# Performance work log

Measured on AMD Instinct MI355X. Metric: run time of the kernel, lower is better.

The kernel has to match this reference:

```python
import jax, jax.numpy as jnp
import numpy as np

PH, PW = 7, 7          # output_size
GRID = 2               # sampling_ratio
SCALES = (0.25, 0.125, 0.0625, 0.03125)  # 2^round(log2(feat/img)) per level
LVL_MIN, LVL_MAX = 2, 5                  # -log2(scales[0]), -log2(scales[-1])
CANON_SCALE, CANON_LVL = 224.0, 4.0
EPS = 1e-6


def setup_inputs() -> dict:
    key = jax.random.key(0)
    ks = jax.random.split(key, 6)
    B, C = 2, 256
    sizes = [(200, 200), (100, 100), (50, 50), (25, 25)]
    inp = {f"feat{i}": jax.random.normal(ks[i], (B, C, h, w), jnp.float32)
           for i, (h, w) in enumerate(sizes)}
    Nb = 256
    # boxes in 800x800 image coords, x1y1 + positive wh so 0<=x1<x2, 0<=y1<y2
    xy = jax.random.uniform(ks[4], (B, Nb, 2), jnp.float32, 0.0, 700.0)
    wh = jax.random.uniform(ks[5], (B, Nb, 2), jnp.float32, 32.0, 512.0)
    inp["boxes"] = jnp.concatenate([xy, xy + wh], axis=-1)
    return inp


def _roi_align_level(feat, b_idx, rois, scale):
    """torchvision roi_align, aligned=False. feat [B,C,H,W], rois [R,4] -> [R,C,PH,PW]."""
    H, W = feat.shape[2], feat.shape[3]
    x1 = rois[:, 0] * scale
    y1 = rois[:, 1] * scale
    x2 = rois[:, 2] * scale
    y2 = rois[:, 3] * scale
    roi_w = jnp.maximum(x2 - x1, 1.0)
    roi_h = jnp.maximum(y2 - y1, 1.0)
    bin_w = roi_w / PW
    bin_h = roi_h / PH
    # sub-bin sampling offsets: (bin + (i+0.5)/grid) for each bin, flattened [PH*GRID]
    gy = (jnp.arange(PH, dtype=jnp.float32)[:, None]
          + (jnp.arange(GRID, dtype=jnp.float32)[None, :] + 0.5) / GRID).reshape(-1)
    gx = (jnp.arange(PW, dtype=jnp.float32)[:, None]
          + (jnp.arange(GRID, dtype=jnp.float32)[None, :] + 0.5) / GRID).reshape(-1)
    ys = y1[:, None] + gy[None, :] * bin_h[:, None]   # [R, PH*G]
    xs = x1[:, None] + gx[None, :] * bin_w[:, None]   # [R, PW*G]
    y = ys[:, :, None]                                 # [R, PH*G, 1]
    x = xs[:, None, :]                                 # [R, 1, PW*G]
    valid = (y >= -1.0) & (y <= H) & (x >= -1.0) & (x <= W)
    yc = jnp.clip(y, 0.0, H - 1)
    xc = jnp.clip(x, 0.0, W - 1)
    yl = jnp.floor(yc).astype(jnp.int32)
    xl = jnp.floor(xc).astype(jnp.int32)
    yh = jnp.minimum(yl + 1, H - 1)
    xh = jnp.minimum(xl + 1, W - 1)
    ly = yc - yl.astype(yc.dtype)
    lx = xc - xl.astype(xc.dtype)
    hy = 1.0 - ly
    hx = 1.0 - lx
    b = b_idx[:, None, None]

    def gather(yi, xi):
        # advanced indexing with slice in channel dim -> [R, PH*G, PW*G, C]
        return feat[b, :, yi, xi]

    val = ((hy * hx)[..., None] * gather(yl, xl)
           + (hy * lx)[..., None] * gather(yl, xh)
           + (ly * hx)[..., None] * gather(yh, xl)
           + (ly * lx)[..., None] * gather(yh, xh))
    val = jnp.where(valid[..., None], val, 0.0)
    R, C = rois.shape[0], feat.shape[1]
    # average over the GRIDxGRID sampling points of each bin
    val = val.reshape(R, PH, GRID, PW, GRID, C).mean(axis=(2, 4))  # [R,PH,PW,C]
    return jnp.transpose(val, (0, 3, 1, 2))                        # [R,C,PH,PW]


def reference(feat0, feat1, feat2, feat3, boxes):
    feats = [feat0, feat1, feat2, feat3]
    B, Nb = boxes.shape[0], boxes.shape[1]
    rois = boxes.reshape(-1, 4)                               # convert_to_roi_format
    b_idx = jnp.repeat(jnp.arange(B), Nb)
    # LevelMapper (FPN eq. 1)
    s = jnp.sqrt(jnp.maximum((rois[:, 2] - rois[:, 0]) * (rois[:, 3] - rois[:, 1]), 0.0))
    lvl = jnp.floor(CANON_LVL + jnp.log2(s / CANON_SCALE + EPS))
    lvl = jnp.clip(lvl, LVL_MIN, LVL_MAX).astype(jnp.int32) - LVL_MIN  # [R] in [0,3]
    out = jnp.zeros((rois.shape[0], feats[0].shape[1], PH, PW), feats[0].dtype)
    for l, (f, sc) in enumerate(zip(feats, SCALES)):
        pooled = _roi_align_level(f, b_idx, rois, sc)
        out = jnp.where((lvl == l)[:, None, None, None], pooled, out)
    return out
```

## Files before the change

### kernel.cpp

```cpp
#include <hip/hip_runtime.h>


#define PHW 49
#define NCHUNK 8
#define CH 32
#define NC 4
#define PSIZE 1024

__global__ __launch_bounds__(256) void msroi_kernel(
    const float* __restrict__ f0, const float* __restrict__ f1,
    const float* __restrict__ f2, const float* __restrict__ f3,
    const float* __restrict__ boxes, float* __restrict__ out)
{
    const int C = 256, Nb = 256;
    const int r = blockIdx.x;
    const int chunk = blockIdx.y;
    const int tid = threadIdx.x;
    const int b = r / Nb;

    const float x1b = boxes[r * 4 + 0];
    const float y1b = boxes[r * 4 + 1];
    const float x2b = boxes[r * 4 + 2];
    const float y2b = boxes[r * 4 + 3];
    const float area = fmaxf((x2b - x1b) * (y2b - y1b), 0.0f);
    const float s = sqrtf(area);
    float lv = floorf(4.0f + log2f(s / 224.0f + 1e-6f));
    lv = fminf(fmaxf(lv, 2.0f), 5.0f);
    const int lvl = (int)lv - 2;

    const float* feat;
    int H, W;
    float scale;
    switch (lvl) {
        case 0:  feat = f0; H = 200; W = 200; scale = 0.25f;    break;
        case 1:  feat = f1; H = 100; W = 100; scale = 0.125f;   break;
        case 2:  feat = f2; H = 50;  W = 50;  scale = 0.0625f;  break;
        default: feat = f3; H = 25;  W = 25;  scale = 0.03125f; break;
    }
    const int HW = H * W;

    const float x1 = x1b * scale, y1 = y1b * scale;
    const float x2 = x2b * scale, y2 = y2b * scale;
    const float roi_w = fmaxf(x2 - x1, 1.0f);
    const float roi_h = fmaxf(y2 - y1, 1.0f);
    const float bin_w = roi_w * (1.0f / 7.0f);
    const float bin_h = roi_h * (1.0f / 7.0f);

    const float ys0 = fminf(fmaxf(y1 + 0.25f * bin_h, 0.0f), (float)(H - 1));
    const float ys1 = fminf(fmaxf(y1 + 6.75f * bin_h, 0.0f), (float)(H - 1));
    const float xs0 = fminf(fmaxf(x1 + 0.25f * bin_w, 0.0f), (float)(W - 1));
    const float xs1 = fminf(fmaxf(x1 + 6.75f * bin_w, 0.0f), (float)(W - 1));
    const int row0 = (int)floorf(ys0);
    const int row1 = min((int)floorf(ys1) + 1, H - 1);
    const int col0 = (int)floorf(xs0);
    const int col1 = min((int)floorf(xs1) + 1, W - 1);
    const int prows = row1 - row0 + 1;
    const int pcols = col1 - col0 + 1;
    const int psize = prows * pcols;
    const int wstride = W - pcols;
    const float inv_pcols = 1.0f / (float)pcols;

    int goff[4];
#pragma unroll
    for (int k = 0; k < 4; ++k) {
        const int e = tid + k * 256;
        const int ec = min(e, psize - 1);
        const int rr = (int)floorf(((float)ec + 0.5f) * inv_pcols);
        goff[k] = ec + rr * wstride;
    }

    const int bin = tid & 63;
    const bool active = bin < PHW;
    int   offs[16];
    float wts[16];
    {
        const int bb = active ? bin : 0;
        const int ph = bb / 7;
        const int pw = bb - ph * 7;
#pragma unroll
        for (int g = 0; g < 4; ++g) {
            const int iy = g >> 1, ix = g & 1;
            const float gy = (float)ph + ((float)iy + 0.5f) * 0.5f;
            const float gx = (float)pw + ((float)ix + 0.5f) * 0.5f;
            const float y = y1 + gy * bin_h;
            const float x = x1 + gx * bin_w;
            const bool valid = (y >= -1.0f) && (y <= (float)H) &&
                               (x >= -1.0f) && (x <= (float)W);
            const float yc = fminf(fmaxf(y, 0.0f), (float)(H - 1));
            const float xc = fminf(fmaxf(x, 0.0f), (float)(W - 1));
            const int yl = (int)floorf(yc);
            const int xl = (int)floorf(xc);
            const int yh = min(yl + 1, H - 1);
            const int xh = min(xl + 1, W - 1);
            const float ly = yc - (float)yl;
            const float lx = xc - (float)xl;
            const float hy = 1.0f - ly, hx = 1.0f - lx;
            const float m = valid ? 0.25f : 0.0f;
            const int ry0 = (yl - row0) * pcols, ry1 = (yh - row0) * pcols;
            const int cx0 = xl - col0, cx1 = xh - col0;
            offs[g * 4 + 0] = ry0 + cx0;  wts[g * 4 + 0] = hy * hx * m;
            offs[g * 4 + 1] = ry0 + cx1;  wts[g * 4 + 1] = hy * lx * m;
            offs[g * 4 + 2] = ry1 + cx0;  wts[g * 4 + 2] = ly * hx * m;
            offs[g * 4 + 3] = ry1 + cx1;  wts[g * 4 + 3] = ly * lx * m;
        }
    }

    __shared__ float lds[NC * PSIZE];
    const int cslot = tid >> 6;
    const int cbase = chunk * CH;
    const float* __restrict__ fch =
        feat + (size_t)(b * C + cbase) * HW + (row0 * W + col0);
    const size_t outBase = (size_t)r * C * PHW + (size_t)cbase * PHW;

    for (int cc = 0; cc < CH; cc += NC) {
        float buf[NC][4];
#pragma unroll
        for (int ch = 0; ch < NC; ++ch) {
            const float* __restrict__ gp = fch + (size_t)(cc + ch) * HW;
#pragma unroll
            for (int k = 0; k < 4; ++k)
                buf[ch][k] = gp[goff[k]];
        }
#pragma unroll
        for (int ch = 0; ch < NC; ++ch) {
#pragma unroll
            for (int k = 0; k < 4; ++k)
                lds[ch * PSIZE + tid + k * 256] = buf[ch][k];
        }
        __syncthreads();

        if (active) {
            const float* __restrict__ p = &lds[cslot * PSIZE];
            float acc = 0.0f;
#pragma unroll
            for (int k = 0; k < 16; ++k)
                acc += wts[k] * p[offs[k]];
            out[outBase + (size_t)(cc + cslot) * PHW + bin] = acc;
        }
        __syncthreads();
    }
}

extern "C" void kernel_launch(void* const* d_in, const int* in_sizes, int n_in,
                              void* d_out, int out_size, void* d_ws, size_t ws_size,
                              hipStream_t stream) {
    const float* f0 = (const float*)d_in[0];
    const float* f1 = (const float*)d_in[1];
    const float* f2 = (const float*)d_in[2];
    const float* f3 = (const float*)d_in[3];
    const float* boxes = (const float*)d_in[4];
    float* out = (float*)d_out;

    const int R = in_sizes[4] / 4;
    dim3 grid(R, NCHUNK);
    msroi_kernel<<<grid, 256, 0, stream>>>(f0, f1, f2, f3, boxes, out);
}
```

Before: 179.6 us.

## Make each wavefront own a channel patch with double-buffered LDS and no barriers

Each 64-lane wavefront now loads the whole ROI patch for its own channel into a private double-buffered LDS slab. It only issues loads up to the actual patch size and prefetches the next channel's patch while computing the current one. This removes the block-wide __syncthreads and the padded-load waste of the old layout, where all 256 threads loaded a shared 4-channel patch together. In exchange it uses twice the LDS (32 KB per block), more registers for the 16-entry offset and buffer arrays, and adds an occupancy hint of 5 blocks per SIMD-unit.

```diff
diff --git a/kernel.cpp b/kernel.cpp
--- a/kernel.cpp
+++ b/kernel.cpp
@@ -4,10 +4,10 @@
 #define PHW 49
 #define NCHUNK 8
 #define CH 32
-#define NC 4
+#define ROUNDS 8
 #define PSIZE 1024
 
-__global__ __launch_bounds__(256) void msroi_kernel(
+__global__ __launch_bounds__(256, 5) void msroi_kernel(
     const float* __restrict__ f0, const float* __restrict__ f1,
     const float* __restrict__ f2, const float* __restrict__ f3,
     const float* __restrict__ boxes, float* __restrict__ out)
@@ -16,6 +16,8 @@
     const int r = blockIdx.x;
     const int chunk = blockIdx.y;
     const int tid = threadIdx.x;
+    const int wv = tid >> 6;
+    const int lane = tid & 63;
     const int b = r / Nb;
 
     const float x1b = boxes[r * 4 + 0];
@@ -59,17 +61,18 @@
     const int psize = prows * pcols;
     const int wstride = W - pcols;
     const float inv_pcols = 1.0f / (float)pcols;
+    const int kmax = (psize + 63) >> 6;
 
-    int goff[4];
+    int goff[16];
 #pragma unroll
-    for (int k = 0; k < 4; ++k) {
-        const int e = tid + k * 256;
+    for (int k = 0; k < 16; ++k) {
+        const int e = lane + k * 64;
         const int ec = min(e, psize - 1);
         const int rr = (int)floorf(((float)ec + 0.5f) * inv_pcols);
         goff[k] = ec + rr * wstride;
     }
 
-    const int bin = tid & 63;
+    const int bin = lane;
     const bool active = bin < PHW;
     int   offs[16];
     float wts[16];
@@ -105,39 +108,42 @@
         }
     }
 
-    __shared__ float lds[NC * PSIZE];
-    const int cslot = tid >> 6;
+    __shared__ float lds[4][2][PSIZE];
+
     const int cbase = chunk * CH;
-    const float* __restrict__ fch =
-        feat + (size_t)(b * C + cbase) * HW + (row0 * W + col0);
+    const float* __restrict__ fwv =
+        feat + (size_t)(b * C + cbase + wv) * HW + (row0 * W + col0);
     const size_t outBase = (size_t)r * C * PHW + (size_t)cbase * PHW;
 
-    for (int cc = 0; cc < CH; cc += NC) {
-        float buf[NC][4];
+    float buf[16];
+
 #pragma unroll
-        for (int ch = 0; ch < NC; ++ch) {
-            const float* __restrict__ gp = fch + (size_t)(cc + ch) * HW;
+    for (int k = 0; k < 16; ++k)
+        if (k < kmax) buf[k] = fwv[goff[k]];
+
 #pragma unroll
-            for (int k = 0; k < 4; ++k)
-                buf[ch][k] = gp[goff[k]];
+    for (int i = 0; i < ROUNDS; ++i) {
+        const int sl = i & 1;
+        float* __restrict__ slab = &lds[wv][sl][0];
+
+#pragma unroll
+        for (int k = 0; k < 16; ++k)
+            if (k < kmax) slab[lane + k * 64] = buf[k];
+
+        if (i + 1 < ROUNDS) {
+            const float* __restrict__ gp = fwv + (size_t)((i + 1) * 4) * HW;
+#pragma unroll
+            for (int k = 0; k < 16; ++k)
+                if (k < kmax) buf[k] = gp[goff[k]];
         }
-#pragma unroll
-        for (int ch = 0; ch < NC; ++ch) {
-#pragma unroll
-            for (int k = 0; k < 4; ++k)
-                lds[ch * PSIZE + tid + k * 256] = buf[ch][k];
-        }
-        __syncthreads();
 
         if (active) {
-            const float* __restrict__ p = &lds[cslot * PSIZE];
             float acc = 0.0f;
 #pragma unroll
             for (int k = 0; k < 16; ++k)
-                acc += wts[k] * p[offs[k]];
-            out[outBase + (size_t)(cc + cslot) * PHW + bin] = acc;
+                acc += wts[k] * slab[offs[k]];
+            out[outBase + (size_t)(i * 4 + wv) * PHW + bin] = acc;
         }
-        __syncthreads();
     }
 }
 
```

After: 186.8 us. 4.0% more time.
